# Kernel tuning notes

Measured on AMD Instinct MI355X. Metric: run time of the kernel, lower is better.

## Reference

```python
import jax, jax.numpy as jnp
import numpy as np

B, S, D, V = 8, 128, 1024, 32000
TEMP, TOP_K, TOP_P = 1.0, 50, 0.95
NEG_INF = jnp.float32(-jnp.inf)


def setup_inputs() -> dict:
    key = jax.random.key(0)
    k1, k2, k3, k4 = jax.random.split(key, 4)
    return {
        "psi_real": jax.random.normal(k1, (B, S, D), dtype=jnp.float32),
        "psi_imag": jax.random.normal(k2, (B, S, D), dtype=jnp.float32),
        "W_r": jax.random.normal(k3, (V, D), dtype=jnp.float32) * (1.0 / np.sqrt(D)),
        "W_i": jax.random.normal(k4, (V, D), dtype=jnp.float32) * (1.0 / np.sqrt(D)),
        "bias": jnp.zeros((V,), dtype=jnp.float32),
    }


def reference(psi_real, psi_imag, W_r, W_i, bias):
    # Complex projection: (psi_r + i psi_i) @ (W_r + i W_i)^T
    amp_r = jnp.einsum("bsd,vd->bsv", psi_real, W_r) - jnp.einsum("bsd,vd->bsv", psi_imag, W_i)
    amp_i = jnp.einsum("bsd,vd->bsv", psi_imag, W_r) + jnp.einsum("bsd,vd->bsv", psi_real, W_i)
    amp_sq = amp_r * amp_r + amp_i * amp_i  # Born rule |amp|^2, [B,S,V]
    floor = jnp.mean(amp_sq, axis=-1, keepdims=True) * 1e-6 + 1e-30
    logits = (jnp.log(amp_sq + floor) + bias) / max(TEMP, 1e-8)
    log_probs = jax.nn.log_softmax(logits, axis=-1)

    # top-k filter: keep values >= k-th largest
    kth = jax.lax.top_k(logits, TOP_K)[0][..., -1:]
    filt = jnp.where(logits < kth, NEG_INF, logits)

    # top-p (nucleus) filter on the top-k-filtered logits
    order = jnp.argsort(-filt, axis=-1)                      # descending sort indices
    sorted_logits = jnp.take_along_axis(filt, order, axis=-1)
    sp = jax.nn.softmax(sorted_logits, axis=-1)
    cum = jnp.cumsum(sp, axis=-1)
    drop = (cum - sp) >= TOP_P                               # cumulative prob excluding current token
    sorted_filt = jnp.where(drop, NEG_INF, sorted_logits)
    inv = jnp.argsort(order, axis=-1)                        # scatter back to original order
    filt2 = jnp.take_along_axis(sorted_filt, inv, axis=-1)

    probs = jax.nn.softmax(filt2, axis=-1)
    tokens = jax.random.categorical(jax.random.key(42), filt2, axis=-1)  # multinomial sample [B,S]
    return logits, log_probs, amp_sq, tokens, probs
```

## Files before the change

### kernel.cpp

```cpp
#include <hip/hip_runtime.h>

#define BS   1024
#define DD   1024
#define VV   32000
#define TOPK 50
#define TOPPF 0.95f
#define NVTOT 32768000ull

typedef __attribute__((ext_vector_type(8)))  short bf16x8;
typedef __attribute__((ext_vector_type(16))) float f32x16;
typedef __attribute__((ext_vector_type(4)))  int   i32x4;

#define MFMA32(A,B,C) __builtin_amdgcn_mfma_f32_32x32x16_bf16(A, B, C, 0, 0, 0)

__device__ __forceinline__ unsigned fkey(float f) {
  unsigned u = __float_as_uint(f);
  return (u & 0x80000000u) ? ~u : (u | 0x80000000u);
}
__device__ __forceinline__ unsigned rotl32(unsigned x, int r) {
  return (x << r) | (x >> (32 - r));
}
__device__ __forceinline__ ushort f2bf(float f) {
  unsigned u = __float_as_uint(f);
  unsigned r = ((u >> 16) & 1u) + 0x7FFFu;
  return (ushort)((u + r) >> 16);
}
__device__ __forceinline__ float bf2f(ushort h) {
  return __uint_as_float(((unsigned)h) << 16);
}
__device__ __forceinline__ bf16x8 negbf(bf16x8 a) {
  i32x4 t = __builtin_bit_cast(i32x4, a);
  t = t ^ 0x80008000;
  return __builtin_bit_cast(bf16x8, t);
}

__device__ float gumbel_at(unsigned i) {
  unsigned x0 = 0u, x1 = i;
  const unsigned ks0 = 0u, ks1 = 42u, ks2 = 0x1BD11BDAu ^ 0u ^ 42u;
  x0 += ks0; x1 += ks1;
  const int rotA[4] = {13, 15, 26, 6};
  const int rotB[4] = {17, 29, 16, 24};
#define TF_R4(R) { x0 += x1; x1 = rotl32(x1, R[0]); x1 ^= x0; \
                   x0 += x1; x1 = rotl32(x1, R[1]); x1 ^= x0; \
                   x0 += x1; x1 = rotl32(x1, R[2]); x1 ^= x0; \
                   x0 += x1; x1 = rotl32(x1, R[3]); x1 ^= x0; }
  TF_R4(rotA); x0 += ks1; x1 += ks2 + 1u;
  TF_R4(rotB); x0 += ks2; x1 += ks0 + 2u;
  TF_R4(rotA); x0 += ks0; x1 += ks1 + 3u;
  TF_R4(rotB); x0 += ks1; x1 += ks2 + 4u;
  TF_R4(rotA); x0 += ks2; x1 += ks0 + 5u;
#undef TF_R4
  unsigned bits = x0 ^ x1;
  float f = __uint_as_float(0x3F800000u | (bits >> 9)) - 1.0f;
  float u = fmaxf(f, 1.17549435e-38f);
  return -logf(-logf(u));
}

__global__ __launch_bounds__(256) void pack_split(
    const float* __restrict__ xr, const float* __restrict__ xi,
    ushort* __restrict__ ohr, ushort* __restrict__ olr,
    ushort* __restrict__ ohi, ushort* __restrict__ oli,
    float si, int n4) {
  int g = blockIdx.x * 256 + threadIdx.x;
  if (g >= n4) return;
  int i = g * 4;
  float4 a = *(const float4*)(xr + i);
  float4 b = *(const float4*)(xi + i);
  float av[4] = {a.x, a.y, a.z, a.w};
  float bv[4] = {b.x * si, b.y * si, b.z * si, b.w * si};
  unsigned hr[4], lr[4], hi_[4], li[4];
#pragma unroll
  for (int j = 0; j < 4; ++j) {
    ushort h = f2bf(av[j]);          hr[j] = h;
    lr[j] = f2bf(av[j] - bf2f(h));
    ushort h2 = f2bf(bv[j]);         hi_[j] = h2;
    li[j] = f2bf(bv[j] - bf2f(h2));
  }
  uint2 w;
  w.x = hr[0] | (hr[1] << 16); w.y = hr[2] | (hr[3] << 16);
  *(uint2*)(ohr + i) = w;
  w.x = lr[0] | (lr[1] << 16); w.y = lr[2] | (lr[3] << 16);
  *(uint2*)(olr + i) = w;
  w.x = hi_[0] | (hi_[1] << 16); w.y = hi_[2] | (hi_[3] << 16);
  *(uint2*)(ohi + i) = w;
  w.x = li[0] | (li[1] << 16); w.y = li[2] | (li[3] << 16);
  *(uint2*)(oli + i) = w;
}

__global__ __launch_bounds__(512, 2) void gemm_mfma(
    const ushort* __restrict__ APk,
    const ushort* __restrict__ Wrh, const ushort* __restrict__ Wrl,
    const ushort* __restrict__ Wih, const ushort* __restrict__ Wil,
    float* __restrict__ amp) {
  __shared__ __align__(16) char lds[2][49152];
  const int tid = threadIdx.x;
  const int lane = tid & 63, wid = tid >> 6;
  const int d = blockIdx.x;
  const int x = d & 7, ii = d >> 3;
  const int bm = x >> 1;
  const int bn = (x & 1) * 125 + ii;
  const int row0 = bm << 8, col0 = bn << 7;
  const int wm = wid >> 1, wn = wid & 1;

  const ushort* tpA[4] = {APk, APk + (1 << 20), APk + (2 << 20), APk + (3 << 20)};
  const ushort* tpB[4] = {Wrh, Wrl, Wih, Wil};

  const int rA = tid >> 1, hA = tid & 1;
  const int sA = hA ^ (rA & 1);
  const int tt = tid >> 8, cb = tid & 255;
  const int rB = cb >> 1, hB = cb & 1;
  const int sB = hB ^ (rB & 1);
  size_t offA[4], offB[2];
#pragma unroll
  for (int t = 0; t < 4; ++t)
    offA[t] = (size_t)(row0 + rA) * DD + (sA << 3);
  offB[0] = (size_t)(col0 + rB) * DD + (sB << 3);
  offB[1] = offB[0];

  f32x16 accr[2][2] = {}, acci[2][2] = {};

  int aoff[2], boff[2];
#pragma unroll
  for (int m = 0; m < 2; ++m) {
    const int ar = (wm << 6) + (m << 5) + (lane & 31);
    aoff[m] = (ar << 5) + (((lane >> 5) ^ (ar & 1)) << 4);
  }
#pragma unroll
  for (int n = 0; n < 2; ++n) {
    const int br = (wn << 6) + (n << 5) + (lane & 31);
    boff[n] = 32768 + (br << 5) + (((lane >> 5) ^ (br & 1)) << 4);
  }

#define STAGE(buf, step) {                                                   \
    const int k0 = (step) << 4;                                              \
    _Pragma("unroll")                                                        \
    for (int t = 0; t < 4; ++t) {                                            \
      __builtin_amdgcn_global_load_lds(                                      \
          (const __attribute__((address_space(1))) unsigned int*)(tpA[t] + offA[t] + k0), \
          (__attribute__((address_space(3))) unsigned int*)                  \
              (&lds[buf][0] + t * 8192 + (tid << 4)),                        \
          16, 0, 0);                                                         \
    }                                                                        \
    _Pragma("unroll")                                                        \
    for (int u = 0; u < 2; ++u) {                                            \
      const int t = (u << 1) + tt;                                           \
      __builtin_amdgcn_global_load_lds(                                      \
          (const __attribute__((address_space(1))) unsigned int*)(tpB[t] + offB[u] + k0), \
          (__attribute__((address_space(3))) unsigned int*)                  \
              (&lds[buf][0] + 32768 + t * 4096 + (cb << 4)),                 \
          16, 0, 0);                                                         \
    }                                                                        \
  }

  STAGE(0, 0);
  __syncthreads();
  for (int step = 0; step < 64; ++step) {
    const int cur = step & 1;
    if (step + 1 < 64) STAGE(cur ^ 1, step + 1);
    const char* Lb = &lds[cur][0];

    bf16x8 bRh[2], bRl[2], bIh[2], bIl[2];
#pragma unroll
    for (int n = 0; n < 2; ++n) {
      bRh[n] = *(const bf16x8*)(Lb + 0 * 4096 + boff[n]);
      bRl[n] = *(const bf16x8*)(Lb + 1 * 4096 + boff[n]);
      bIh[n] = *(const bf16x8*)(Lb + 2 * 4096 + boff[n]);
      bIl[n] = *(const bf16x8*)(Lb + 3 * 4096 + boff[n]);
    }
#pragma unroll
    for (int m = 0; m < 2; ++m) {
      bf16x8 aPrh = *(const bf16x8*)(Lb + 0 * 8192 + aoff[m]);
      bf16x8 aPrl = *(const bf16x8*)(Lb + 1 * 8192 + aoff[m]);
      bf16x8 aNih = *(const bf16x8*)(Lb + 2 * 8192 + aoff[m]);
      bf16x8 aNil = *(const bf16x8*)(Lb + 3 * 8192 + aoff[m]);
      bf16x8 aPih = negbf(aNih);
      bf16x8 aPil = negbf(aNil);
#pragma unroll
      for (int n = 0; n < 2; ++n) {
        f32x16 r = accr[m][n], q = acci[m][n];
        r = MFMA32(aPrh, bRh[n], r); r = MFMA32(aPrh, bRl[n], r); r = MFMA32(aPrl, bRh[n], r);
        r = MFMA32(aNih, bIh[n], r); r = MFMA32(aNih, bIl[n], r); r = MFMA32(aNil, bIh[n], r);
        q = MFMA32(aPih, bRh[n], q); q = MFMA32(aPih, bRl[n], q); q = MFMA32(aPil, bRh[n], q);
        q = MFMA32(aPrh, bIh[n], q); q = MFMA32(aPrh, bIl[n], q); q = MFMA32(aPrl, bIh[n], q);
        accr[m][n] = r; acci[m][n] = q;
      }
    }
    __syncthreads();
  }
#undef STAGE
#pragma unroll
  for (int m = 0; m < 2; ++m)
#pragma unroll
    for (int n = 0; n < 2; ++n) {
      f32x16 r = accr[m][n], q = acci[m][n];
      const int colg = col0 + (wn << 6) + (n << 5) + (lane & 31);
      const int rowb = row0 + (wm << 6) + (m << 5) + ((lane >> 5) << 2);
#pragma unroll
      for (int reg = 0; reg < 16; ++reg) {
        const int row = rowb + (reg & 3) + ((reg >> 2) << 3);
        float vr = r[reg], vi = q[reg];
        amp[(size_t)row * VV + colg] = vr * vr + vi * vi;
      }
    }
}

__global__ __launch_bounds__(512) void post_row(
    const float* __restrict__ amp, const float* __restrict__ bias,
    float* __restrict__ logits, float* __restrict__ logprobs,
    float* __restrict__ probs, float* __restrict__ tokens) {
  __shared__ __align__(16) float lg[VV];
  __shared__ int hist[4096];
  __shared__ int iscan[512];
  __shared__ float red[512];
  __shared__ float sval[768]; __shared__ int sidx[768];
  __shared__ float ssv[768];  __shared__ int ssi[768];
  __shared__ int scnt;
  __shared__ float sh_f[4];
  __shared__ int   sh_i[4];

  const int row = blockIdx.x, tid = threadIdx.x;
  const float* A = amp + (size_t)row * VV;
  float* Lg = logits + (size_t)row * VV;
  float* Lp = logprobs + (size_t)row * VV;
  float* P  = probs + (size_t)row * VV;

  float s = 0.f;
  for (int i = tid; i < VV / 4; i += 512) {
    float4 a = ((const float4*)A)[i];
    ((float4*)lg)[i] = a;
    s += a.x + a.y + a.z + a.w;
  }
  red[tid] = s; __syncthreads();
  for (int o = 256; o > 0; o >>= 1) { if (tid < o) red[tid] += red[tid + o]; __syncthreads(); }
  if (tid == 0) sh_f[0] = red[0] * (1.0f / (float)VV) * 1e-6f + 1e-30f;
  __syncthreads();
  const float floorv = sh_f[0];
  __syncthreads();

  float mx = -INFINITY;
  for (int i = tid; i < VV / 4; i += 512) {
    float4 a = ((float4*)lg)[i];
    float4 b = ((const float4*)bias)[i];
    float4 l;
    l.x = logf(a.x + floorv) + b.x;
    l.y = logf(a.y + floorv) + b.y;
    l.z = logf(a.z + floorv) + b.z;
    l.w = logf(a.w + floorv) + b.w;
    ((float4*)lg)[i] = l;
    ((float4*)Lg)[i] = l;
    mx = fmaxf(mx, fmaxf(fmaxf(l.x, l.y), fmaxf(l.z, l.w)));
  }
  red[tid] = mx; __syncthreads();
  for (int o = 256; o > 0; o >>= 1) { if (tid < o) red[tid] = fmaxf(red[tid], red[tid + o]); __syncthreads(); }
  mx = red[0]; __syncthreads();

  float se = 0.f;
  for (int i = tid; i < VV / 4; i += 512) {
    float4 l = ((float4*)lg)[i];
    se += expf(l.x - mx) + expf(l.y - mx) + expf(l.z - mx) + expf(l.w - mx);
  }
  red[tid] = se; __syncthreads();
  for (int o = 256; o > 0; o >>= 1) { if (tid < o) red[tid] += red[tid + o]; __syncthreads(); }
  const float lse = mx + logf(red[0]);
  __syncthreads();

  for (int i = tid; i < VV / 4; i += 512) {
    float4 l = ((float4*)lg)[i];
    float4 o4 = {l.x - lse, l.y - lse, l.z - lse, l.w - lse};
    ((float4*)Lp)[i] = o4;
  }

  for (int i = tid; i < 4096; i += 512) hist[i] = 0;
  if (tid == 0) scnt = 0;
  __syncthreads();
  for (int v = tid; v < VV; v += 512)
    atomicAdd(&hist[fkey(lg[v]) >> 20], 1);
  __syncthreads();
  {
    const int hi = 4095 - 8 * tid;
    int part = 0;
#pragma unroll
    for (int j = 0; j < 8; ++j) part += hist[hi - j];
    iscan[tid] = part;
    __syncthreads();
    for (int off = 1; off < 512; off <<= 1) {
      int add = (tid >= off) ? iscan[tid - off] : 0;
      __syncthreads();
      iscan[tid] += add;
      __syncthreads();
    }
    int cum = iscan[tid], prev = tid ? iscan[tid - 1] : 0;
    if (cum >= TOPK && prev < TOPK) sh_i[0] = tid;
    __syncthreads();
    if (tid == 0) {
      int tc = sh_i[0];
      int c = tc ? iscan[tc - 1] : 0;
      int b = 4095 - 8 * tc;
      for (int j = 0; j < 8; ++j) {
        int h = hist[4095 - 8 * tc - j];
        if (c + h >= TOPK) { b = 4095 - 8 * tc - j; break; }
        c += h;
      }
      sh_i[1] = b;
    }
    __syncthreads();
  }
  const unsigned binb = (unsigned)sh_i[1];

  for (int v = tid; v < VV; v += 512) {
    if ((fkey(lg[v]) >> 20) >= binb) {
      int p = atomicAdd(&scnt, 1);
      if (p < 768) { sval[p] = lg[v]; sidx[p] = v; }
    }
  }
  __syncthreads();
  const int n = min(scnt, 768);
  for (int i = tid; i < n; i += 512) {
    float vi = sval[i]; int ii = sidx[i]; int r = 0;
    for (int j = 0; j < n; ++j) {
      float vj = sval[j]; int ij = sidx[j];
      r += (vj > vi) || (vj == vi && ij < ii);
    }
    ssv[r] = vi; ssi[r] = ii;
  }
  __syncthreads();
  if (tid == 0) {
    const float kthv = ssv[TOPK - 1];
    int np = TOPK;
    while (np < n && ssv[np] >= kthv) ++np;
    const float mx2 = ssv[0];
    float denom = 0.f;
    for (int j = 0; j < np; ++j) denom += expf(ssv[j] - mx2);
    float cum = 0.f; int m = np;
    for (int j = 0; j < np; ++j) {
      float sp = expf(ssv[j] - mx2) / denom;
      cum += sp;
      if (cum - sp >= TOPPF) { m = j; break; }
    }
    float dk = 0.f;
    for (int j = 0; j < m; ++j) dk += expf(ssv[j] - mx2);
    sh_f[1] = mx2; sh_f[2] = dk; sh_f[3] = ssv[m - 1];
    sh_i[2] = ssi[m - 1];
  }
  __syncthreads();
  const float mx2 = sh_f[1], dk = sh_f[2], vb = sh_f[3];
  const int ib = sh_i[2];

  float best = -INFINITY; int bidx = 0x7FFFFFFF;
  for (int i = tid; i < VV / 4; i += 512) {
    float4 l4 = ((float4*)lg)[i];
    float lv[4] = {l4.x, l4.y, l4.z, l4.w};
    float4 p4 = {0.f, 0.f, 0.f, 0.f};
    float pv[4] = {0.f, 0.f, 0.f, 0.f};
#pragma unroll
    for (int j = 0; j < 4; ++j) {
      const int v = i * 4 + j;
      float l = lv[j];
      bool kept = (l > vb) || (l == vb && v <= ib);
      if (kept) {
        pv[j] = expf(l - mx2) / dk;
        float g = gumbel_at((unsigned)(row * VV + v));
        float sc = l + g;
        if (sc > best || (sc == best && v < bidx)) { best = sc; bidx = v; }
      }
    }
    p4.x = pv[0]; p4.y = pv[1]; p4.z = pv[2]; p4.w = pv[3];
    ((float4*)P)[i] = p4;
  }
  red[tid] = best; iscan[tid] = bidx; __syncthreads();
  for (int o = 256; o > 0; o >>= 1) {
    if (tid < o) {
      if (red[tid + o] > red[tid] ||
          (red[tid + o] == red[tid] && iscan[tid + o] < iscan[tid])) {
        red[tid] = red[tid + o]; iscan[tid] = iscan[tid + o];
      }
    }
    __syncthreads();
  }
  if (tid == 0) tokens[row] = (float)iscan[0];
}

extern "C" void kernel_launch(void* const* d_in, const int* in_sizes, int n_in,
                              void* d_out, int out_size, void* d_ws, size_t ws_size,
                              hipStream_t stream) {
  const float* pr   = (const float*)d_in[0];
  const float* pi   = (const float*)d_in[1];
  const float* wr   = (const float*)d_in[2];
  const float* wi   = (const float*)d_in[3];
  const float* bias = (const float*)d_in[4];

  float* out      = (float*)d_out;
  float* logits   = out;
  float* logprobs = out + NVTOT;
  float* ampsq    = out + 2 * NVTOT;
  float* tokens   = out + 3 * NVTOT;
  float* probs    = out + 3 * NVTOT + 1024;

  ushort* Wrh = (ushort*)logits;
  ushort* Wrl = Wrh + 32768000;
  ushort* Wih = (ushort*)logprobs;
  ushort* Wil = Wih + 32768000;
  ushort* APk = (ushort*)probs;

  pack_split<<<1024, 256, 0, stream>>>(pr, pi,
      APk, APk + (1 << 20), APk + (2 << 20), APk + (3 << 20), -1.0f, 262144);
  pack_split<<<32000, 256, 0, stream>>>(wr, wi,
      Wrh, Wrl, Wih, Wil, 1.0f, 8192000);

  gemm_mfma<<<1000, 512, 0, stream>>>(APk, Wrh, Wrl, Wih, Wil, ampsq);

  post_row<<<BS, 512, 0, stream>>>(ampsq, bias, logits, logprobs, probs, tokens);
}
```

Baseline: 1.064 ms.

## Split GEMM staging into two phases with explicit vmcnt waits and MFMA priority

Reorganizes the bf16-split complex GEMM main loop so global-to-LDS loads for the next K step go out in two halves, interleaved between the two M sub-tile compute phases. Explicit s_waitcnt vmcnt and s_barrier replace __syncthreads, and s_setprio raises wave priority around the MFMA chains. The LDS layout changes from the XOR-swizzled interleaved form to a k-half-major layout, which changes bank access patterns. The aims are better overlap of memory latency with MFMA work and less barrier stall. The risks are LDS bank conflicts from the unswizzled layout and subtle hazards from the hand-placed waits.

```diff
diff --git a/kernel.cpp b/kernel.cpp
--- a/kernel.cpp
+++ b/kernel.cpp
@@ -105,17 +105,13 @@
   const ushort* tpA[4] = {APk, APk + (1 << 20), APk + (2 << 20), APk + (3 << 20)};
   const ushort* tpB[4] = {Wrh, Wrl, Wih, Wil};
 
-  const int rA = tid >> 1, hA = tid & 1;
-  const int sA = hA ^ (rA & 1);
+  const int rowA = tid & 255, khA = tid >> 8;
+  const size_t srcA = (size_t)(row0 + rowA) * DD + (khA << 3);
   const int tt = tid >> 8, cb = tid & 255;
-  const int rB = cb >> 1, hB = cb & 1;
-  const int sB = hB ^ (rB & 1);
-  size_t offA[4], offB[2];
-#pragma unroll
-  for (int t = 0; t < 4; ++t)
-    offA[t] = (size_t)(row0 + rA) * DD + (sA << 3);
-  offB[0] = (size_t)(col0 + rB) * DD + (sB << 3);
-  offB[1] = offB[0];
+  const int rowB = cb & 127, khB = cb >> 7;
+  const size_t srcB = (size_t)(col0 + rowB) * DD + (khB << 3);
+  const int dstA = tid << 4;
+  const int dstB = cb << 4;
 
   f32x16 accr[2][2] = {}, acci[2][2] = {};
 
@@ -123,42 +119,44 @@
 #pragma unroll
   for (int m = 0; m < 2; ++m) {
     const int ar = (wm << 6) + (m << 5) + (lane & 31);
-    aoff[m] = (ar << 5) + (((lane >> 5) ^ (ar & 1)) << 4);
+    aoff[m] = ((lane >> 5) << 12) + (ar << 4);
   }
 #pragma unroll
   for (int n = 0; n < 2; ++n) {
     const int br = (wn << 6) + (n << 5) + (lane & 31);
-    boff[n] = 32768 + (br << 5) + (((lane >> 5) ^ (br & 1)) << 4);
-  }
-
-#define STAGE(buf, step) {                                                   \
+    boff[n] = 32768 + ((lane >> 5) << 11) + (br << 4);
+  }
+
+#define GLDS(src, dst) __builtin_amdgcn_global_load_lds(                     \
+      (const __attribute__((address_space(1))) unsigned int*)(src),          \
+      (__attribute__((address_space(3))) unsigned int*)(dst), 16, 0, 0)
+
+#define STAGE_P0(buf, step) {                                                \
     const int k0 = (step) << 4;                                              \
-    _Pragma("unroll")                                                        \
-    for (int t = 0; t < 4; ++t) {                                            \
-      __builtin_amdgcn_global_load_lds(                                      \
-          (const __attribute__((address_space(1))) unsigned int*)(tpA[t] + offA[t] + k0), \
-          (__attribute__((address_space(3))) unsigned int*)                  \
-              (&lds[buf][0] + t * 8192 + (tid << 4)),                        \
-          16, 0, 0);                                                         \
-    }                                                                        \
-    _Pragma("unroll")                                                        \
-    for (int u = 0; u < 2; ++u) {                                            \
-      const int t = (u << 1) + tt;                                           \
-      __builtin_amdgcn_global_load_lds(                                      \
-          (const __attribute__((address_space(1))) unsigned int*)(tpB[t] + offB[u] + k0), \
-          (__attribute__((address_space(3))) unsigned int*)                  \
-              (&lds[buf][0] + 32768 + t * 4096 + (cb << 4)),                 \
-          16, 0, 0);                                                         \
-    }                                                                        \
-  }
-
-  STAGE(0, 0);
-  __syncthreads();
+    GLDS(tpA[0] + srcA + k0, &lds[buf][0] + 0 * 8192 + dstA);                \
+    GLDS(tpA[1] + srcA + k0, &lds[buf][0] + 1 * 8192 + dstA);                \
+    GLDS(tpB[tt] + srcB + k0, &lds[buf][0] + 32768 + tt * 4096 + dstB);      \
+  }
+#define STAGE_P1(buf, step) {                                                \
+    const int k0 = (step) << 4;                                              \
+    GLDS(tpA[2] + srcA + k0, &lds[buf][0] + 2 * 8192 + dstA);                \
+    GLDS(tpA[3] + srcA + k0, &lds[buf][0] + 3 * 8192 + dstA);                \
+    GLDS(tpB[2 + tt] + srcB + k0, &lds[buf][0] + 32768 + (2 + tt) * 4096 + dstB); \
+  }
+
+  STAGE_P0(0, 0);
+  STAGE_P1(0, 0);
   for (int step = 0; step < 64; ++step) {
     const int cur = step & 1;
-    if (step + 1 < 64) STAGE(cur ^ 1, step + 1);
+    if (step + 1 < 64) {
+      STAGE_P0(cur ^ 1, step + 1);
+      asm volatile("s_waitcnt vmcnt(3)" ::: "memory");
+    } else {
+      asm volatile("s_waitcnt vmcnt(0)" ::: "memory");
+    }
+    asm volatile("s_barrier" ::: "memory");
+
     const char* Lb = &lds[cur][0];
-
     bf16x8 bRh[2], bRl[2], bIh[2], bIl[2];
 #pragma unroll
     for (int n = 0; n < 2; ++n) {
@@ -167,27 +165,51 @@
       bIh[n] = *(const bf16x8*)(Lb + 2 * 4096 + boff[n]);
       bIl[n] = *(const bf16x8*)(Lb + 3 * 4096 + boff[n]);
     }
-#pragma unroll
-    for (int m = 0; m < 2; ++m) {
-      bf16x8 aPrh = *(const bf16x8*)(Lb + 0 * 8192 + aoff[m]);
-      bf16x8 aPrl = *(const bf16x8*)(Lb + 1 * 8192 + aoff[m]);
-      bf16x8 aNih = *(const bf16x8*)(Lb + 2 * 8192 + aoff[m]);
-      bf16x8 aNil = *(const bf16x8*)(Lb + 3 * 8192 + aoff[m]);
+    {
+      bf16x8 aPrh = *(const bf16x8*)(Lb + 0 * 8192 + aoff[0]);
+      bf16x8 aPrl = *(const bf16x8*)(Lb + 1 * 8192 + aoff[0]);
+      bf16x8 aNih = *(const bf16x8*)(Lb + 2 * 8192 + aoff[0]);
+      bf16x8 aNil = *(const bf16x8*)(Lb + 3 * 8192 + aoff[0]);
       bf16x8 aPih = negbf(aNih);
       bf16x8 aPil = negbf(aNil);
+      __builtin_amdgcn_s_setprio(1);
 #pragma unroll
       for (int n = 0; n < 2; ++n) {
-        f32x16 r = accr[m][n], q = acci[m][n];
+        f32x16 r = accr[0][n], q = acci[0][n];
         r = MFMA32(aPrh, bRh[n], r); r = MFMA32(aPrh, bRl[n], r); r = MFMA32(aPrl, bRh[n], r);
         r = MFMA32(aNih, bIh[n], r); r = MFMA32(aNih, bIl[n], r); r = MFMA32(aNil, bIh[n], r);
         q = MFMA32(aPih, bRh[n], q); q = MFMA32(aPih, bRl[n], q); q = MFMA32(aPil, bRh[n], q);
         q = MFMA32(aPrh, bIh[n], q); q = MFMA32(aPrh, bIl[n], q); q = MFMA32(aPrl, bIh[n], q);
-        accr[m][n] = r; acci[m][n] = q;
-      }
-    }
-    __syncthreads();
-  }
-#undef STAGE
+        accr[0][n] = r; acci[0][n] = q;
+      }
+      __builtin_amdgcn_s_setprio(0);
+    }
+    asm volatile("s_barrier" ::: "memory");
+    if (step + 1 < 64) STAGE_P1(cur ^ 1, step + 1);
+    {
+      bf16x8 aPrh = *(const bf16x8*)(Lb + 0 * 8192 + aoff[1]);
+      bf16x8 aPrl = *(const bf16x8*)(Lb + 1 * 8192 + aoff[1]);
+      bf16x8 aNih = *(const bf16x8*)(Lb + 2 * 8192 + aoff[1]);
+      bf16x8 aNil = *(const bf16x8*)(Lb + 3 * 8192 + aoff[1]);
+      bf16x8 aPih = negbf(aNih);
+      bf16x8 aPil = negbf(aNil);
+      __builtin_amdgcn_s_setprio(1);
+#pragma unroll
+      for (int n = 0; n < 2; ++n) {
+        f32x16 r = accr[1][n], q = acci[1][n];
+        r = MFMA32(aPrh, bRh[n], r); r = MFMA32(aPrh, bRl[n], r); r = MFMA32(aPrl, bRh[n], r);
+        r = MFMA32(aNih, bIh[n], r); r = MFMA32(aNih, bIl[n], r); r = MFMA32(aNil, bIh[n], r);
+        q = MFMA32(aPih, bRh[n], q); q = MFMA32(aPih, bRl[n], q); q = MFMA32(aPil, bRh[n], q);
+        q = MFMA32(aPrh, bIh[n], q); q = MFMA32(aPrh, bIl[n], q); q = MFMA32(aPrl, bIh[n], q);
+        accr[1][n] = r; acci[1][n] = q;
+      }
+      __builtin_amdgcn_s_setprio(0);
+    }
+    asm volatile("s_barrier" ::: "memory");
+  }
+#undef STAGE_P0
+#undef STAGE_P1
+#undef GLDS
 #pragma unroll
   for (int m = 0; m < 2; ++m)
 #pragma unroll
```

Result: slower. 1.149 ms (+8.0%).
